# Kernel optimization log

Measured on AMD Instinct MI355X. Metric: run time of the kernel, lower is better.

The kernel has to match this reference:

```python
import jax, jax.numpy as jnp
import numpy as np
import math

EMSIZE = 512
NX = 2048        # emsize * (layer_id+1), layer_id=3
H = NX // EMSIZE # 4 heads of size EMSIZE (grow_head path)
B, S = 4, 2048
EPS = 1e-5


def _layernorm(x, g, b):
    u = jnp.mean(x, axis=-1, keepdims=True)
    s = jnp.mean((x - u) ** 2, axis=-1, keepdims=True)
    return g * (x - u) / jnp.sqrt(s + EPS) + b


def _gelu(x):
    # OpenAI tanh-approx gelu, exactly as in source
    return 0.5 * x * (1.0 + jnp.tanh(jnp.sqrt(2.0 / jnp.pi) * (x + 0.044715 * x ** 3)))


def setup_inputs() -> dict:
    key = jax.random.key(0)
    ks = jax.random.split(key, 8)
    std = 0.02
    return {
        "x": jax.random.normal(ks[0], (B, S, NX), jnp.float32),
        "w_qkv": jax.random.normal(ks[1], (NX, 3 * NX), jnp.float32) * std,
        "b_qkv": jnp.zeros((3 * NX,), jnp.float32),
        "w_ao": jax.random.normal(ks[2], (NX, NX), jnp.float32) * std,
        "b_ao": jnp.zeros((NX,), jnp.float32),
        "ln1_g": jnp.ones((NX,), jnp.float32),
        "ln1_b": jnp.zeros((NX,), jnp.float32),
        "w_fc": jax.random.normal(ks[3], (NX, 4 * NX), jnp.float32) * std,
        "b_fc": jnp.zeros((4 * NX,), jnp.float32),
        "w_pr": jax.random.normal(ks[4], (4 * NX, NX), jnp.float32) * std,
        "b_pr": jnp.zeros((NX,), jnp.float32),
        "ln2_g": jnp.ones((NX,), jnp.float32),
        "ln2_b": jnp.zeros((NX,), jnp.float32),
        "w_out": jax.random.normal(ks[5], (NX, EMSIZE), jnp.float32) * std,
        "b_out": jnp.zeros((EMSIZE,), jnp.float32),
    }


def reference(x, w_qkv, b_qkv, w_ao, b_ao, ln1_g, ln1_b, w_fc, b_fc,
              w_pr, b_pr, ln2_g, ln2_b, w_out, b_out):
    Bx, Sx, _ = x.shape
    # --- multi-head attention ---
    qkv = x @ w_qkv + b_qkv                       # [B,S,3*NX]
    q, k, v = jnp.split(qkv, 3, axis=-1)
    q = q.reshape(Bx, Sx, H, EMSIZE).transpose(0, 2, 1, 3)  # [B,H,S,E]
    k = k.reshape(Bx, Sx, H, EMSIZE).transpose(0, 2, 1, 3)
    v = v.reshape(Bx, Sx, H, EMSIZE).transpose(0, 2, 1, 3)
    w = jnp.einsum("bhqe,bhke->bhqk", q, k) / jnp.sqrt(jnp.float32(EMSIZE))
    alen = jnp.arange(Sx)
    mask = alen[None, :] <= alen[:, None]          # causal [S,S]
    # source: w*mask + -1e9*(1-mask) == where(mask, w, -1e9)
    w = jnp.where(mask[None, None], w, jnp.float32(-1e9))
    w = jax.nn.softmax(w, axis=-1)
    a = jnp.einsum("bhqk,bhke->bhqe", w, v)        # [B,H,S,E]
    a = a.transpose(0, 2, 1, 3).reshape(Bx, Sx, NX)
    a = a @ w_ao + b_ao
    # --- residual + LN + MLP + LN ---
    n = _layernorm(x + a, ln1_g, ln1_b)
    m = (_gelu(n @ w_fc + b_fc)) @ w_pr + b_pr
    h = _layernorm(n + m, ln2_g, ln2_b)
    # --- final projection + grow_head concat ---
    h = h @ w_out + b_out                          # [B,S,EMSIZE]
    h = h.reshape(Bx, Sx, 1, EMSIZE)
    j = x.reshape(Bx, Sx, H, EMSIZE)
    out = jnp.concatenate([j, h], axis=-2)         # [B,S,H+1,E]
    return out.reshape(Bx, Sx, (H + 1) * EMSIZE)
```

## Files before the change

kernel.cpp:

```cpp
#include <hip/hip_runtime.h>
#include <hip/hip_bf16.h>
#include <math.h>

using bf16 = __hip_bfloat16;
typedef __attribute__((ext_vector_type(8))) short s16x8;
typedef __attribute__((ext_vector_type(4))) float f32x4;

struct __align__(16) B8 { bf16 v[8]; };
struct __align__(8)  B4 { bf16 v[4]; };

__device__ __forceinline__ float b2f(bf16 x){ return __bfloat162float(x); }
__device__ __forceinline__ bf16  f2b(float x){ return __float2bfloat16(x); }

enum { EPI_QKV=0, EPI_AO=3, EPI_FC=4, EPI_PRB=5, EPI_OUT=6 };

#define SCHED0 __builtin_amdgcn_sched_barrier(0)
#define PRIO1  __builtin_amdgcn_s_setprio(1)
#define PRIO0  __builtin_amdgcn_s_setprio(0)
#define BAR    __builtin_amdgcn_s_barrier()
#define VM6    asm volatile("s_waitcnt vmcnt(6)" ::: "memory")
#define VM4    asm volatile("s_waitcnt vmcnt(4)" ::: "memory")
#define VM2    asm volatile("s_waitcnt vmcnt(2)" ::: "memory")
#define VM0    asm volatile("s_waitcnt vmcnt(0)" ::: "memory")
#define LGKM0  asm volatile("s_waitcnt lgkmcnt(0)" ::: "memory")
#define AS1    const __attribute__((address_space(1))) void*
#define AS3    __attribute__((address_space(3))) void*

template<int EPI>
__launch_bounds__(512, 2)
__global__ void gemm256(const bf16* __restrict__ A, const bf16* __restrict__ B,
                        void* __restrict__ Cv, const float* __restrict__ bias,
                        const void* __restrict__ res,
                        int K, int lda, int ldb, int ldc, int ldres, int nbx)
{
    extern __shared__ __align__(16) bf16 lds[];
    bf16* Asl = lds;
    bf16* Bsl = lds + 32768;

    const int nwg = (int)gridDim.x;
    int wg = (int)blockIdx.x;
    if ((nwg & 7) == 0) wg = (wg & 7)*(nwg >> 3) + (wg >> 3);
    const int bx = wg % nbx, by = wg / nbx;
    const long m0 = (long)by*256, n0 = (long)bx*256;

    const int tid = threadIdx.x, wave = tid>>6, lane = tid&63;
    const int wr = wave>>2, wc = wave&3;
    const int NT = K>>6;
    const int fr = lane&15, fg = lane>>4;

    const int ck0 = fg ^ (fr&7);
    const int ck1 = (4+fg) ^ (fr&7);
    const bf16* aRd0 = Asl + wr*4096 + fr*64 + ck0*8;
    const bf16* aRd1 = Asl + wr*4096 + fr*64 + ck1*8;
    const bf16* bRd0 = Bsl + wc*2048 + fr*64 + ck0*8;
    const bf16* bRd1 = Bsl + wc*2048 + fr*64 + ck1*8;

    #define RDA(d, rh) { _Pragma("unroll") for (int i=0;i<4;++i){ \
        a[i][0] = *(const s16x8*)(aRd0 + (d)*16384 + (rh)*8192 + i*1024); \
        a[i][1] = *(const s16x8*)(aRd1 + (d)*16384 + (rh)*8192 + i*1024); } }
    #define RDB(dst, d, ch) { _Pragma("unroll") for (int j=0;j<2;++j){ \
        dst[j][0] = *(const s16x8*)(bRd0 + (d)*16384 + (ch)*8192 + j*1024); \
        dst[j][1] = *(const s16x8*)(bRd1 + (d)*16384 + (ch)*8192 + j*1024); } }

    const int grow = tid>>3;
    const int gc0  = (tid&7) ^ (grow&7);
    const bf16* aP = A + (m0 + grow)*(long)lda + gc0*8;
    const bf16* bP = B + (n0 + grow)*(long)ldb + gc0*8;

    #define STGA(sd, sh, koff) { _Pragma("unroll") for (int l=0;l<2;++l) \
        __builtin_amdgcn_global_load_lds((AS1)(aP + ((sh)*128 + l*64)*(long)lda + (koff)), \
            (AS3)(Asl + (sd)*16384 + (sh)*8192 + l*4096 + wave*512 + lane*8), 16, 0, 0); }
    #define STGB(sd, sh, koff) { _Pragma("unroll") for (int l=0;l<2;++l) \
        __builtin_amdgcn_global_load_lds((AS1)(bP + ((sh)*128 + l*64)*(long)ldb + (koff)), \
            (AS3)(Bsl + (sd)*16384 + (sh)*8192 + l*4096 + wave*512 + lane*8), 16, 0, 0); }

    f32x4 acc[2][4][2][2];
    #pragma unroll
    for (int rh=0;rh<2;++rh)
        #pragma unroll
        for (int i=0;i<4;++i)
            #pragma unroll
            for (int ch=0;ch<2;++ch)
                #pragma unroll
                for (int j=0;j<2;++j)
                    #pragma unroll
                    for (int r=0;r<4;++r) acc[rh][i][ch][j][r] = 0.f;

    #define MM(rh, ch, BB) { PRIO1; \
        _Pragma("unroll") for (int i=0;i<4;++i) \
        _Pragma("unroll") for (int j=0;j<2;++j) \
        _Pragma("unroll") for (int kk=0;kk<2;++kk) \
            acc[rh][i][ch][j] = __builtin_amdgcn_mfma_f32_16x16x32_bf16(a[i][kk], BB[j][kk], acc[rh][i][ch][j], 0,0,0); \
        PRIO0; }

    s16x8 a[4][2], b0[2][2], b1[2][2];

    STGA(0,0,0);  STGB(0,1,0);  STGA(0,1,0);  STGB(0,0,0);
    STGA(1,0,64); STGB(1,1,64); STGA(1,1,64);
    VM6; SCHED0; BAR;

    for (int t=0; t<=NT-4; t+=2){
        RDB(b0,0,0); RDA(0,0); STGB(1,0,64);
        SCHED0; BAR; LGKM0; MM(0,0,b0); SCHED0; BAR;
        RDB(b1,0,1);           STGA(0,0,128);
        SCHED0; BAR; LGKM0; MM(0,1,b1); SCHED0; BAR;
        RDA(0,1);              STGB(0,1,128);
        SCHED0; BAR; LGKM0; MM(1,1,b1); SCHED0; BAR;
                               STGA(0,1,128); VM6;
        SCHED0; BAR; LGKM0; MM(1,0,b0); SCHED0; BAR;
        RDB(b0,1,0); RDA(1,0); STGB(0,0,128);
        SCHED0; BAR; LGKM0; MM(0,0,b0); SCHED0; BAR;
        RDB(b1,1,1);           STGA(1,0,192);
        SCHED0; BAR; LGKM0; MM(0,1,b1); SCHED0; BAR;
        RDA(1,1);              STGB(1,1,192);
        SCHED0; BAR; LGKM0; MM(1,1,b1); SCHED0; BAR;
                               STGA(1,1,192); VM6;
        SCHED0; BAR; LGKM0; MM(1,0,b0); SCHED0; BAR;
        aP += 128; bP += 128;
    }

    RDB(b0,0,0); RDA(0,0); STGB(1,0,64);
    SCHED0; BAR; LGKM0; MM(0,0,b0); SCHED0; BAR;
    RDB(b1,0,1);
    SCHED0; BAR; LGKM0; MM(0,1,b1); SCHED0; BAR;
    RDA(0,1);
    SCHED0; BAR; LGKM0; MM(1,1,b1); SCHED0; BAR;
    VM0;
    SCHED0; BAR; LGKM0; MM(1,0,b0); SCHED0; BAR;
    RDB(b0,1,0); RDA(1,0);
    SCHED0; BAR; LGKM0; MM(0,0,b0); SCHED0; BAR;
    RDB(b1,1,1);
    SCHED0; BAR; LGKM0; MM(0,1,b1); SCHED0; BAR;
    RDA(1,1);
    SCHED0; BAR; LGKM0; MM(1,1,b1); SCHED0; BAR;
    MM(1,0,b0);

    #undef RDA
    #undef RDB
    #undef STGA
    #undef STGB
    #undef MM

    #pragma unroll
    for (int rh=0;rh<2;++rh)
        #pragma unroll
        for (int i=0;i<4;++i)
            #pragma unroll
            for (int ch=0;ch<2;++ch)
                #pragma unroll
                for (int j=0;j<2;++j)
                    #pragma unroll
                    for (int r=0;r<4;++r){
                        const long mm = m0 + rh*128 + wr*64 + i*16 + fg*4 + r;
                        const long nn = n0 + ch*128 + wc*32 + j*16 + fr;
                        const float v = acc[rh][i][ch][j][r];
                        if constexpr (EPI==EPI_AO){
                            ((float*)Cv)[mm*ldc + nn] = v + bias[nn] + ((const float*)res)[mm*ldres + nn];
                        } else if constexpr (EPI==EPI_PRB){
                            ((bf16*)Cv)[mm*ldc + nn] = f2b(v + bias[nn] + b2f(((const bf16*)res)[mm*ldres + nn]));
                        } else if constexpr (EPI==EPI_FC){
                            const float tt = v + bias[nn];
                            const float g = 0.5f*tt*(1.f + tanhf(0.7978845608028654f*(tt + 0.044715f*tt*tt*tt)));
                            ((bf16*)Cv)[mm*ldc + nn] = f2b(g);
                        } else if constexpr (EPI==EPI_OUT){
                            ((float*)Cv)[mm*ldc + nn] = v + bias[nn];
                        } else {
                            ((bf16*)Cv)[mm*ldc + nn] = f2b(v + bias[nn]);
                        }
                    }
}

__launch_bounds__(512, 2)
__global__ void fattn(const bf16* __restrict__ qkv, const bf16* __restrict__ vt,
                      bf16* __restrict__ outp)
{
    extern __shared__ __align__(16) bf16 sh[];
    bf16* sQ = sh;
    bf16* sK = sh + 32768;
    bf16* sP = sh + 57344;
    bf16* sV = sh + 65536;
    float* part = (float*)(sh + 32768);

    const int bid = blockIdx.x;
    const int xcd = bid&7, t5 = bid>>3, rnd = t5>>5, ci = t5&31;
    const int bh = xcd*2 + rnd, b = bh>>2, h = bh&3;
    const int ib = 31 - ci;
    const int njb = (ib>>1) + 1;
    const int tid = threadIdx.x, wave = tid>>6, lane = tid&63;
    const int wr = wave>>2, wc = wave&3;
    const int fr = lane&15, fg = lane>>4;

    const bf16* Qg = qkv + ((long)b*2048 + ib*64)*6144 + h*512;
    const bf16* Kg = qkv + (long)b*2048*6144 + 2048 + h*512;
    const bf16* Vtb = vt + (long)bh*1048576;
    const float SCALE = 0.044194173824159216f;

    #define STGQ { _Pragma("unroll") for (int l=0;l<8;++l){                          \
        const int row = l*8 + (tid>>6);                                              \
        const int c   = (tid&63) ^ (row&7);                                          \
        __builtin_amdgcn_global_load_lds((AS1)(Qg + (long)row*6144 + c*8),           \
            (AS3)(sQ + l*4096 + wave*512 + lane*8), 16,0,0); } }
    #define STGK(slot, ec, KJ) { _Pragma("unroll") for (int l=0;l<2;++l){            \
        const int row = l*64 + (tid>>3);                                             \
        const int c   = (tid&7) ^ (row&7);                                           \
        __builtin_amdgcn_global_load_lds((AS1)((KJ) + (long)row*6144 + (ec)*64 + c*8),\
            (AS3)(sK + (slot)*8192 + l*4096 + wave*512 + lane*8), 16,0,0); } }
    #define STGV(buf, kf, eh, VJ) { _Pragma("unroll") for (int l=0;l<2;++l){         \
        const int row = l*128 + (tid>>2);                                            \
        const int c   = (tid&3) ^ ((row + (row>>2))&3);                              \
        __builtin_amdgcn_global_load_lds((AS1)((VJ) + (long)((eh)*256+row)*2048 + (kf)*32 + c*8),\
            (AS3)(sV + (buf)*8192 + l*4096 + wave*512 + lane*8), 16,0,0); } }

    f32x4 acc[2][8];
    #pragma unroll
    for (int m=0;m<2;++m)
        #pragma unroll
        for (int j=0;j<8;++j)
            #pragma unroll
            for (int r=0;r<4;++r) acc[m][j][r] = 0.f;
    float l_l[2][4];
    #pragma unroll
    for (int m=0;m<2;++m){ l_l[m][0]=0.f; l_l[m][1]=0.f; l_l[m][2]=0.f; l_l[m][3]=0.f; }

    const bf16* KgJ = Kg;
    const bf16* VtJ = Vtb;

    STGQ;
    STGK(0, 0, KgJ);
    STGK(1, 1, KgJ);
    VM2; SCHED0; BAR;

    for (int jb=0; jb<njb; ++jb){
        const bool last = (jb == njb-1);
        f32x4 sacc[2][2];
        #pragma unroll
        for (int m=0;m<2;++m)
            #pragma unroll
            for (int nf=0;nf<2;++nf)
                #pragma unroll
                for (int r=0;r<4;++r) sacc[m][nf][r] = 0.f;

        #pragma unroll
        for (int ec=0; ec<8; ++ec){
            const int slot = ec%3;
            s16x8 qa[2][2], kb[2][2];
            #pragma unroll
            for (int m=0;m<2;++m)
                #pragma unroll
                for (int kk=0;kk<2;++kk){
                    const int row = wr*32 + m*16 + fr;
                    const int c = (ec*2+kk)*4 + fg;
                    qa[m][kk] = *(const s16x8*)(sQ + row*512 + ((c ^ (row&7))*8));
                }
            #pragma unroll
            for (int nf=0;nf<2;++nf)
                #pragma unroll
                for (int kk=0;kk<2;++kk){
                    const int row = wc*32 + nf*16 + fr;
                    const int c = kk*4 + fg;
                    kb[nf][kk] = *(const s16x8*)(sK + slot*8192 + row*64 + ((c ^ (row&7))*8));
                }
            if (ec < 6) STGK((ec+2)%3, ec+2, KgJ);
            PRIO1;
            #pragma unroll
            for (int m=0;m<2;++m)
                #pragma unroll
                for (int nf=0;nf<2;++nf)
                    #pragma unroll
                    for (int kk=0;kk<2;++kk)
                        sacc[m][nf] = __builtin_amdgcn_mfma_f32_16x16x32_bf16(qa[m][kk], kb[nf][kk], sacc[m][nf], 0,0,0);
            PRIO0;
            if (ec < 6) { VM2; } else if (ec == 6) { VM0; }
            SCHED0; BAR;
        }

        const int doff = (njb-1)*128 - ib*64;
        #pragma unroll
        for (int m=0;m<2;++m)
            #pragma unroll
            for (int nf=0;nf<2;++nf)
                #pragma unroll
                for (int r=0;r<4;++r){
                    float pv = __expf(sacc[m][nf][r]*SCALE - 4.0f);
                    const int rl = wr*32 + m*16 + fg*4 + r;
                    const int cl = wc*32 + nf*16 + fr;
                    if (last && (cl + doff > rl)) pv = 0.f;
                    sP[rl*128 + (((cl>>3) ^ (rl&15))*8) + (cl&7)] = f2b(pv);
                    l_l[m][r] += pv;
                }
        STGV(0, 0, 0, VtJ);
        if (!last){ STGK(0, 0, KgJ + 786432); STGK(1, 1, KgJ + 786432); }
        if (!last){ VM4; } else { VM0; }
        LGKM0; SCHED0; BAR;

        s16x8 pa[2];
        #pragma unroll
        for (int v=0; v<8; ++v){
            const int kf = v>>1, eh = v&1, buf = v&1;
            if (eh == 0){
                #pragma unroll
                for (int m=0;m<2;++m){
                    const int row = wr*32 + m*16 + fr;
                    const int c = kf*4 + fg;
                    pa[m] = *(const s16x8*)(sP + row*128 + ((c ^ (row&15))*8));
                }
            }
            s16x8 vb[4];
            #pragma unroll
            for (int nf=0;nf<4;++nf){
                const int row = wc*64 + nf*16 + fr;
                vb[nf] = *(const s16x8*)(sV + buf*8192 + row*32 + (((fg ^ ((row + (row>>2))&3)))*8));
            }
            if (v < 7) STGV((v+1)&1, (v+1)>>1, (v+1)&1, VtJ);
            PRIO1;
            #pragma unroll
            for (int m=0;m<2;++m)
                #pragma unroll
                for (int nf=0;nf<4;++nf)
                    acc[m][eh*4+nf] = __builtin_amdgcn_mfma_f32_16x16x32_bf16(pa[m], vb[nf], acc[m][eh*4+nf], 0,0,0);
            PRIO0;
            if (v < 7) { VM0; }
            SCHED0; BAR;
        }
        KgJ += 786432;
        VtJ += 128;
    }

    #pragma unroll
    for (int m=0;m<2;++m)
        #pragma unroll
        for (int r=0;r<4;++r){
            float v = l_l[m][r];
            v += __shfl_xor(v, 1); v += __shfl_xor(v, 2);
            v += __shfl_xor(v, 4); v += __shfl_xor(v, 8);
            l_l[m][r] = v;
        }
    if (fr == 0){
        #pragma unroll
        for (int m=0;m<2;++m)
            #pragma unroll
            for (int r=0;r<4;++r)
                part[(wr*32 + m*16 + fg*4 + r)*4 + wc] = l_l[m][r];
    }
    LGKM0; SCHED0; BAR;

    bf16* orow = outp + ((long)b*2048 + ib*64)*2048 + h*512;
    #pragma unroll
    for (int m=0;m<2;++m)
        #pragma unroll
        for (int r=0;r<4;++r){
            const int rl = wr*32 + m*16 + fg*4 + r;
            const f32x4 pp = *(const f32x4*)(part + rl*4);
            const float rinv = 1.f/(pp[0]+pp[1]+pp[2]+pp[3]);
            #pragma unroll
            for (int j=0;j<8;++j){
                const int e = (j>>2)*256 + wc*64 + (j&3)*16 + fr;
                orow[(long)rl*2048 + e] = f2b(acc[m][j][r]*rinv);
            }
        }
    #undef STGQ
    #undef STGK
    #undef STGV
}

__launch_bounds__(256)
__global__ void wtrans(const float* __restrict__ W, bf16* __restrict__ Wt, int Kd, int Nd){
    __shared__ float t[32][33];
    const int n0 = blockIdx.x*32, k0 = blockIdx.y*32;
    const int tx = threadIdx.x&31, ty = threadIdx.x>>5;
    #pragma unroll
    for (int i=0;i<32;i+=8) t[ty+i][tx] = W[(long)(k0+ty+i)*Nd + n0+tx];
    __syncthreads();
    #pragma unroll
    for (int i=0;i<32;i+=8) Wt[(long)(n0+ty+i)*Kd + k0+tx] = f2b(t[tx][ty+i]);
}

__launch_bounds__(256)
__global__ void vtrans(const bf16* __restrict__ qkv, bf16* __restrict__ vt){
    const int z = blockIdx.z, b = z>>2, h = z&3;
    const bf16* in = qkv + (long)b*12582912 + 4096 + h*512;
    bf16* outp = vt + (long)z*1048576;
    __shared__ bf16 t[32][33];
    const int e0 = blockIdx.x*32, s0 = blockIdx.y*32;
    const int tx = threadIdx.x&31, ty = threadIdx.x>>5;
    #pragma unroll
    for (int i=0;i<32;i+=8) t[ty+i][tx] = in[(long)(s0+ty+i)*6144 + e0+tx];
    __syncthreads();
    #pragma unroll
    for (int i=0;i<32;i+=8) outp[(long)(e0+ty+i)*2048 + s0+tx] = t[tx][ty+i];
}

__launch_bounds__(256)
__global__ void cvt_f32_bf16(const float* __restrict__ in, bf16* __restrict__ outp){
    const long i = ((long)blockIdx.x*256 + threadIdx.x)*4;
    const float4 v = *(const float4*)&in[i];
    B4 o; o.v[0]=f2b(v.x); o.v[1]=f2b(v.y); o.v[2]=f2b(v.z); o.v[3]=f2b(v.w);
    *reinterpret_cast<B4*>(&outp[i]) = o;
}

__launch_bounds__(256)
__global__ void jcopy(const float* __restrict__ x, float* __restrict__ outp){
    const long idx = ((long)blockIdx.x*256 + threadIdx.x)*4;
    const long r = idx>>11, c = idx&2047;
    *(float4*)&outp[r*2560 + c] = *(const float4*)&x[idx];
}

template<int BF>
__launch_bounds__(256)
__global__ void ln_rows(const void* __restrict__ inp, const float* __restrict__ gw,
                        const float* __restrict__ bw, bf16* __restrict__ outp){
    const long r = blockIdx.x;
    const int tid = threadIdx.x, k0 = tid*8;
    float v[8];
    if constexpr (BF){
        const bf16* row = (const bf16*)inp + r*2048;
        const B8 x = *reinterpret_cast<const B8*>(&row[k0]);
        #pragma unroll
        for (int i=0;i<8;++i) v[i] = b2f(x.v[i]);
    } else {
        const float* row = (const float*)inp + r*2048;
        const float4 a = *(const float4*)&row[k0];
        const float4 c = *(const float4*)&row[k0+4];
        v[0]=a.x; v[1]=a.y; v[2]=a.z; v[3]=a.w; v[4]=c.x; v[5]=c.y; v[6]=c.z; v[7]=c.w;
    }
    float s = 0.f, qq = 0.f;
    #pragma unroll
    for (int i=0;i<8;++i){ s += v[i]; qq += v[i]*v[i]; }
    #pragma unroll
    for (int o=32;o;o>>=1){ s += __shfl_xor(s,o); qq += __shfl_xor(qq,o); }
    __shared__ float s1[4], s2[4];
    if ((tid&63)==0){ s1[tid>>6]=s; s2[tid>>6]=qq; }
    __syncthreads();
    s  = s1[0]+s1[1]+s1[2]+s1[3];
    qq = s2[0]+s2[1]+s2[2]+s2[3];
    const float mean = s*(1.f/2048.f);
    const float var  = qq*(1.f/2048.f) - mean*mean;
    const float rinv = rsqrtf(var + 1e-5f);
    const float4 g1 = *(const float4*)&gw[k0];
    const float4 g2 = *(const float4*)&gw[k0+4];
    const float4 b1 = *(const float4*)&bw[k0];
    const float4 b2 = *(const float4*)&bw[k0+4];
    const float gg[8] = {g1.x,g1.y,g1.z,g1.w,g2.x,g2.y,g2.z,g2.w};
    const float bb[8] = {b1.x,b1.y,b1.z,b1.w,b2.x,b2.y,b2.z,b2.w};
    B8 o;
    #pragma unroll
    for (int i=0;i<8;++i) o.v[i] = f2b((v[i]-mean)*rinv*gg[i] + bb[i]);
    *reinterpret_cast<B8*>(&outp[r*2048 + k0]) = o;
}

extern "C" void kernel_launch(void* const* d_in, const int* in_sizes, int n_in,
                              void* d_out, int out_size, void* d_ws, size_t ws_size,
                              hipStream_t stream)
{
    (void)in_sizes; (void)n_in; (void)out_size;
    const float* x     = (const float*)d_in[0];
    const float* w_qkv = (const float*)d_in[1];
    const float* b_qkv = (const float*)d_in[2];
    const float* w_ao  = (const float*)d_in[3];
    const float* b_ao  = (const float*)d_in[4];
    const float* ln1g  = (const float*)d_in[5];
    const float* ln1b  = (const float*)d_in[6];
    const float* w_fc  = (const float*)d_in[7];
    const float* b_fc  = (const float*)d_in[8];
    const float* w_pr  = (const float*)d_in[9];
    const float* b_pr  = (const float*)d_in[10];
    const float* ln2g  = (const float*)d_in[11];
    const float* ln2b  = (const float*)d_in[12];
    const float* w_out = (const float*)d_in[13];
    const float* b_out = (const float*)d_in[14];
    float* out = (float*)d_out;
    char* ws = (char*)d_ws;

    const size_t NEEDED = 245366784ull;
    if (ws_size < NEEDED) return;

    bf16*  xb     = (bf16*)(ws);
    bf16*  qkv    = (bf16*)(ws + 33554432ull);
    float* r1     = (float*)(ws + 33554432ull);
    bf16*  fcact  = (bf16*)(ws);
    bf16*  vt     = (bf16*)(ws + 134217728ull);
    bf16*  Wfc_t  = (bf16*)(ws + 134217728ull);
    bf16*  rbufB  = (bf16*)(ws + 134217728ull);
    bf16*  Wpr_t  = (bf16*)(ws + 167772160ull);
    bf16*  Wqkv_t = (bf16*)(ws + 201326592ull);
    bf16*  nbuf   = (bf16*)(ws + 201326592ull);
    bf16*  Wao_t  = (bf16*)(ws + 234881024ull);
    bf16*  Wout_t = (bf16*)(ws + 243269632ull);

    const dim3 T(256);
    const int SMEM = 131072;
    const int SMEM_A = 163840;
    (void)hipFuncSetAttribute((const void*)gemm256<EPI_QKV>, hipFuncAttributeMaxDynamicSharedMemorySize, SMEM);
    (void)hipFuncSetAttribute((const void*)gemm256<EPI_AO>,  hipFuncAttributeMaxDynamicSharedMemorySize, SMEM);
    (void)hipFuncSetAttribute((const void*)gemm256<EPI_FC>,  hipFuncAttributeMaxDynamicSharedMemorySize, SMEM);
    (void)hipFuncSetAttribute((const void*)gemm256<EPI_PRB>, hipFuncAttributeMaxDynamicSharedMemorySize, SMEM);
    (void)hipFuncSetAttribute((const void*)gemm256<EPI_OUT>, hipFuncAttributeMaxDynamicSharedMemorySize, SMEM);
    (void)hipFuncSetAttribute((const void*)fattn,            hipFuncAttributeMaxDynamicSharedMemorySize, SMEM_A);

    wtrans<<<dim3(192,64),T,0,stream>>>(w_qkv, Wqkv_t, 2048, 6144);
    wtrans<<<dim3(64,64), T,0,stream>>>(w_ao,  Wao_t,  2048, 2048);
    wtrans<<<dim3(16,64), T,0,stream>>>(w_out, Wout_t, 2048, 512);
    cvt_f32_bf16<<<16384,T,0,stream>>>(x, xb);

    gemm256<EPI_QKV><<<dim3(768),dim3(512),SMEM,stream>>>(xb, Wqkv_t, qkv, b_qkv, nullptr,
        2048, 2048, 2048, 6144, 0, 24);
    vtrans<<<dim3(16,64,16),T,0,stream>>>(qkv, vt);

    fattn<<<dim3(512),dim3(512),SMEM_A,stream>>>(qkv, vt, xb);

    gemm256<EPI_AO><<<dim3(256),dim3(512),SMEM,stream>>>(xb, Wao_t, r1, b_ao, x,
        2048, 2048, 2048, 2048, 2048, 8);
    ln_rows<0><<<8192,T,0,stream>>>(r1, ln1g, ln1b, nbuf);

    wtrans<<<dim3(256,64),T,0,stream>>>(w_fc, Wfc_t, 2048, 8192);
    wtrans<<<dim3(64,256),T,0,stream>>>(w_pr, Wpr_t, 8192, 2048);
    gemm256<EPI_FC><<<dim3(1024),dim3(512),SMEM,stream>>>(nbuf, Wfc_t, fcact, b_fc, nullptr,
        2048, 2048, 2048, 8192, 0, 32);
    gemm256<EPI_PRB><<<dim3(256),dim3(512),SMEM,stream>>>(fcact, Wpr_t, rbufB, b_pr, nbuf,
        8192, 8192, 8192, 2048, 2048, 8);
    ln_rows<1><<<8192,T,0,stream>>>(rbufB, ln2g, ln2b, nbuf);

    gemm256<EPI_OUT><<<dim3(64),dim3(512),SMEM,stream>>>(nbuf, Wout_t, out + 2048, b_out, nullptr,
        2048, 2048, 2048, 2560, 0, 2);
    jcopy<<<16384,T,0,stream>>>(x, out);
}
```

Before: 1.080 ms.

## Split-K the final output projection and drop sched barriers in GEMM loop

The final projection GEMM (M=8192, N=512, K=2048) launched only 64 workgroups; it now splits K into four slices across blockIdx.y, writes fp32 partials to workspace, and a new reduction kernel sums them with the bias into the output. The aim is to fill more compute units for this small-N GEMM, at the cost of extra partial-sum traffic and one more launch. Separately, the sched_barrier(0) fences around the MFMA phases are removed from all gemm256 instances, which gives the compiler more freedom to interleave instructions but may disturb the hand-tuned schedule.

```diff
diff --git a/kernel.cpp b/kernel.cpp
--- a/kernel.cpp
+++ b/kernel.cpp
@@ -43,6 +43,12 @@
     const int bx = wg % nbx, by = wg / nbx;
     const long m0 = (long)by*256, n0 = (long)bx*256;
 
+    if constexpr (EPI==EPI_OUT){
+        const long ko = (long)blockIdx.y * K;
+        A += ko; B += ko;
+        Cv = (void*)((float*)Cv + (long)blockIdx.y * 4194304);
+    }
+
     const int tid = threadIdx.x, wave = tid>>6, lane = tid&63;
     const int wr = wave>>2, wc = wave&3;
     const int NT = K>>6;
@@ -97,42 +103,42 @@
 
     STGA(0,0,0);  STGB(0,1,0);  STGA(0,1,0);  STGB(0,0,0);
     STGA(1,0,64); STGB(1,1,64); STGA(1,1,64);
-    VM6; SCHED0; BAR;
+    VM6; BAR;
 
     for (int t=0; t<=NT-4; t+=2){
         RDB(b0,0,0); RDA(0,0); STGB(1,0,64);
-        SCHED0; BAR; LGKM0; MM(0,0,b0); SCHED0; BAR;
+        BAR; LGKM0; MM(0,0,b0); BAR;
         RDB(b1,0,1);           STGA(0,0,128);
-        SCHED0; BAR; LGKM0; MM(0,1,b1); SCHED0; BAR;
+        BAR; LGKM0; MM(0,1,b1); BAR;
         RDA(0,1);              STGB(0,1,128);
-        SCHED0; BAR; LGKM0; MM(1,1,b1); SCHED0; BAR;
+        BAR; LGKM0; MM(1,1,b1); BAR;
                                STGA(0,1,128); VM6;
-        SCHED0; BAR; LGKM0; MM(1,0,b0); SCHED0; BAR;
+        BAR; LGKM0; MM(1,0,b0); BAR;
         RDB(b0,1,0); RDA(1,0); STGB(0,0,128);
-        SCHED0; BAR; LGKM0; MM(0,0,b0); SCHED0; BAR;
+        BAR; LGKM0; MM(0,0,b0); BAR;
         RDB(b1,1,1);           STGA(1,0,192);
-        SCHED0; BAR; LGKM0; MM(0,1,b1); SCHED0; BAR;
+        BAR; LGKM0; MM(0,1,b1); BAR;
         RDA(1,1);              STGB(1,1,192);
-        SCHED0; BAR; LGKM0; MM(1,1,b1); SCHED0; BAR;
+        BAR; LGKM0; MM(1,1,b1); BAR;
                                STGA(1,1,192); VM6;
-        SCHED0; BAR; LGKM0; MM(1,0,b0); SCHED0; BAR;
+        BAR; LGKM0; MM(1,0,b0); BAR;
         aP += 128; bP += 128;
     }
 
     RDB(b0,0,0); RDA(0,0); STGB(1,0,64);
-    SCHED0; BAR; LGKM0; MM(0,0,b0); SCHED0; BAR;
+    BAR; LGKM0; MM(0,0,b0); BAR;
     RDB(b1,0,1);
-    SCHED0; BAR; LGKM0; MM(0,1,b1); SCHED0; BAR;
+    BAR; LGKM0; MM(0,1,b1); BAR;
     RDA(0,1);
-    SCHED0; BAR; LGKM0; MM(1,1,b1); SCHED0; BAR;
+    BAR; LGKM0; MM(1,1,b1); BAR;
     VM0;
-    SCHED0; BAR; LGKM0; MM(1,0,b0); SCHED0; BAR;
+    BAR; LGKM0; MM(1,0,b0); BAR;
     RDB(b0,1,0); RDA(1,0);
-    SCHED0; BAR; LGKM0; MM(0,0,b0); SCHED0; BAR;
+    BAR; LGKM0; MM(0,0,b0); BAR;
     RDB(b1,1,1);
-    SCHED0; BAR; LGKM0; MM(0,1,b1); SCHED0; BAR;
+    BAR; LGKM0; MM(0,1,b1); BAR;
     RDA(1,1);
-    SCHED0; BAR; LGKM0; MM(1,1,b1); SCHED0; BAR;
+    BAR; LGKM0; MM(1,1,b1); BAR;
     MM(1,0,b0);
 
     #undef RDA
@@ -163,11 +169,26 @@
                             const float g = 0.5f*tt*(1.f + tanhf(0.7978845608028654f*(tt + 0.044715f*tt*tt*tt)));
                             ((bf16*)Cv)[mm*ldc + nn] = f2b(g);
                         } else if constexpr (EPI==EPI_OUT){
-                            ((float*)Cv)[mm*ldc + nn] = v + bias[nn];
+                            ((float*)Cv)[mm*ldc + nn] = v;
                         } else {
                             ((bf16*)Cv)[mm*ldc + nn] = f2b(v + bias[nn]);
                         }
                     }
+}
+
+__launch_bounds__(256)
+__global__ void kred(const float* __restrict__ p, const float* __restrict__ bias,
+                     float* __restrict__ outp){
+    const long idx = ((long)blockIdx.x*256 + threadIdx.x)*4;
+    const long r = idx>>9, c = idx&511;
+    float4 s0 = *(const float4*)&p[idx];
+    const float4 s1 = *(const float4*)&p[idx + 4194304];
+    const float4 s2 = *(const float4*)&p[idx + 8388608];
+    const float4 s3 = *(const float4*)&p[idx + 12582912];
+    const float4 bb = *(const float4*)&bias[c];
+    s0.x += s1.x+s2.x+s3.x+bb.x; s0.y += s1.y+s2.y+s3.y+bb.y;
+    s0.z += s1.z+s2.z+s3.z+bb.z; s0.w += s1.w+s2.w+s3.w+bb.w;
+    *(float4*)&outp[r*2560 + 2048 + c] = s0;
 }
 
 __launch_bounds__(512, 2)
@@ -478,6 +499,7 @@
     bf16*  qkv    = (bf16*)(ws + 33554432ull);
     float* r1     = (float*)(ws + 33554432ull);
     bf16*  fcact  = (bf16*)(ws);
+    float* kpart  = (float*)(ws);
     bf16*  vt     = (bf16*)(ws + 134217728ull);
     bf16*  Wfc_t  = (bf16*)(ws + 134217728ull);
     bf16*  rbufB  = (bf16*)(ws + 134217728ull);
@@ -520,7 +542,8 @@
         8192, 8192, 8192, 2048, 2048, 8);
     ln_rows<1><<<8192,T,0,stream>>>(rbufB, ln2g, ln2b, nbuf);
 
-    gemm256<EPI_OUT><<<dim3(64),dim3(512),SMEM,stream>>>(nbuf, Wout_t, out + 2048, b_out, nullptr,
-        2048, 2048, 2048, 2560, 0, 2);
+    gemm256<EPI_OUT><<<dim3(64,4),dim3(512),SMEM,stream>>>(nbuf, Wout_t, kpart, nullptr, nullptr,
+        512, 2048, 2048, 512, 0, 2);
+    kred<<<4096,T,0,stream>>>(kpart, b_out, out);
     jcopy<<<16384,T,0,stream>>>(x, out);
 }
```

Measured after the change: 1.065 ms. Within noise of the previous version (-1.4%).
